# Kernel tuning notes

Hardware: AMD Instinct MI355X
Metric: run time of the kernel (lower is better)

## Reference

```python
import jax, jax.numpy as jnp
import numpy as np

H = 128  # hidden_size

def setup_inputs() -> dict:
    key = jax.random.key(0)
    ks = jax.random.split(key, 12)
    B, SEQ = 256, 1000
    static = jax.random.normal(ks[0], (B, 2, SEQ), jnp.float32)
    dynamic = jax.random.uniform(ks[1], (B, 2, SEQ), jnp.float32)
    # Encoder = 1x1 Conv1d(in_ch -> H): weight (H, in_ch), bias (H,)
    def xavier(k, shape):
        fan_in, fan_out = shape[1], shape[0]
        lim = np.sqrt(6.0 / (fan_in + fan_out)).astype(np.float32)
        return jax.random.uniform(k, shape, jnp.float32, -lim, lim)
    enc_s_w = xavier(ks[2], (H, 2)); enc_s_b = jnp.zeros((H,), jnp.float32)
    enc_d_w = xavier(ks[3], (H, 2)); enc_d_b = jnp.zeros((H,), jnp.float32)
    v = xavier(ks[4], (1, H))[0]                 # attention vector (H,)
    W = xavier(ks[5], (H, 3 * H))                # attention matrix (H, 3H)
    dense_w = xavier(ks[6], (H, 128)); dense_b = jnp.zeros((H,), jnp.float32)
    lin_w = xavier(ks[7], (1, H)); lin_b = jnp.zeros((1,), jnp.float32)
    return {"static": static, "dynamic": dynamic,
            "enc_s_w": enc_s_w, "enc_s_b": enc_s_b,
            "enc_d_w": enc_d_w, "enc_d_b": enc_d_b,
            "v": v, "W": W,
            "dense_w": dense_w, "dense_b": dense_b,
            "lin_w": lin_w, "lin_b": lin_b}


def reference(static, dynamic, enc_s_w, enc_s_b, enc_d_w, enc_d_b,
              v, W, dense_w, dense_b, lin_w, lin_b):
    B = static.shape[0]
    # 1x1-conv encoders (computed once; identical across loop iterations)
    e = jnp.einsum('hc,bcs->bhs', enc_s_w, static) + enc_s_b[None, :, None]   # (B,H,S)
    dyn_ld = jnp.broadcast_to(dynamic[:, 1:2, :], dynamic.shape)              # load channel expanded
    d = jnp.einsum('hc,bcs->bhs', enc_d_w, dyn_ld) + enc_d_b[None, :, None]   # (B,H,S)
    hy = jnp.zeros((B, H), static.dtype)
    for _ in range(3):  # fixed 3-step refinement loop
        hidden = jnp.concatenate(
            [e, d, jnp.broadcast_to(hy[:, :, None], e.shape)], axis=1)        # (B,3H,S)
        u = jnp.tanh(jnp.einsum('hk,bks->bhs', W, hidden))                    # (B,H,S)
        logit = jnp.einsum('h,bhs->bs', v, u)                                 # (B,S)
        prob = jax.nn.softmax(logit, axis=-1)
        hy = jnp.einsum('bs,bhs->bh', prob, e)                                # context update
    out = jax.nn.relu(hy @ dense_w.T + dense_b) @ lin_w.T + lin_b             # (B,1)
    return out
```

## Files before the change

kernel.cpp:

```cpp
#include <hip/hip_runtime.h>
#include <math.h>

#define HH 128
#define SS 1000
#define NT 1024
#define NW (NT / 64)
#define PCT 512

#define C1 2.8853900817779268f
#define C2 1.4426950408889634f

__global__ __launch_bounds__(PCT) void sc_precompute(
    const float* __restrict__ enc_s_w, const float* __restrict__ enc_s_b,
    const float* __restrict__ enc_d_w, const float* __restrict__ enc_d_b,
    const float* __restrict__ v, const float* __restrict__ W,
    float* __restrict__ ws) {
    __shared__ float part[7][4][HH];
    const int t = threadIdx.x;
    const int h = t & (HH - 1);
    const int q = t >> 7;
    const float4* W1 = (const float4*)(W + h * (3 * HH));
    const float4* W2 = (const float4*)(W + h * (3 * HH) + HH);
    const float4* W3 = (const float4*)(W + h * (3 * HH) + 2 * HH);
    const float4* ES = (const float4*)enc_s_w;
    const float4* ED = (const float4*)enc_d_w;
    const float4* SB = (const float4*)enc_s_b;
    const float4* DB = (const float4*)enc_d_b;
    float a0 = 0.f, a1 = 0.f, ad = 0.f, cc = 0.f, w30 = 0.f, w31 = 0.f, w3b = 0.f;
    #pragma unroll
    for (int k4 = q * 8; k4 < q * 8 + 8; ++k4) {
        float4 w1 = W1[k4], w2 = W2[k4], w3 = W3[k4];
        float4 e01 = ES[2 * k4], e23 = ES[2 * k4 + 1];
        float4 d01 = ED[2 * k4], d23 = ED[2 * k4 + 1];
        float4 sb = SB[k4], db = DB[k4];
        a0 = fmaf(w1.x, e01.x, a0); a0 = fmaf(w1.y, e01.z, a0);
        a0 = fmaf(w1.z, e23.x, a0); a0 = fmaf(w1.w, e23.z, a0);
        a1 = fmaf(w1.x, e01.y, a1); a1 = fmaf(w1.y, e01.w, a1);
        a1 = fmaf(w1.z, e23.y, a1); a1 = fmaf(w1.w, e23.w, a1);
        ad = fmaf(w2.x, d01.x + d01.y, ad); ad = fmaf(w2.y, d01.z + d01.w, ad);
        ad = fmaf(w2.z, d23.x + d23.y, ad); ad = fmaf(w2.w, d23.z + d23.w, ad);
        cc = fmaf(w1.x, sb.x, cc); cc = fmaf(w1.y, sb.y, cc);
        cc = fmaf(w1.z, sb.z, cc); cc = fmaf(w1.w, sb.w, cc);
        cc = fmaf(w2.x, db.x, cc); cc = fmaf(w2.y, db.y, cc);
        cc = fmaf(w2.z, db.z, cc); cc = fmaf(w2.w, db.w, cc);
        w30 = fmaf(w3.x, e01.x, w30); w30 = fmaf(w3.y, e01.z, w30);
        w30 = fmaf(w3.z, e23.x, w30); w30 = fmaf(w3.w, e23.z, w30);
        w31 = fmaf(w3.x, e01.y, w31); w31 = fmaf(w3.y, e01.w, w31);
        w31 = fmaf(w3.z, e23.y, w31); w31 = fmaf(w3.w, e23.w, w31);
        w3b = fmaf(w3.x, sb.x, w3b); w3b = fmaf(w3.y, sb.y, w3b);
        w3b = fmaf(w3.z, sb.z, w3b); w3b = fmaf(w3.w, sb.w, w3b);
    }
    part[0][q][h] = a0;  part[1][q][h] = a1;  part[2][q][h] = ad;
    part[3][q][h] = cc;  part[4][q][h] = w30; part[5][q][h] = w31;
    part[6][q][h] = w3b;
    __syncthreads();
    if (t < HH) {
        float r[7];
        #pragma unroll
        for (int i = 0; i < 7; ++i)
            r[i] = (part[i][0][t] + part[i][1][t]) + (part[i][2][t] + part[i][3][t]);
        ws[t]           = r[0] * C1;
        ws[HH + t]      = r[1] * C1;
        ws[2 * HH + t]  = r[2] * C1;
        ws[3 * HH + t]  = v[t];
        ws[4 * HH + t]  = r[3] * C1;
        ws[5 * HH + t]  = (r[3] + r[6]) * C1;
        ws[6 * HH + t]  = r[4] * C1;
        ws[7 * HH + t]  = r[5] * C1;
    }
    if (t == 0) {
        const float4* V4 = (const float4*)v;
        float s = 0.f;
        #pragma unroll 4
        for (int k = 0; k < HH / 4; ++k) { float4 x = V4[k]; s += x.x + x.y + x.z + x.w; }
        ws[8 * HH] = s * C2;
    }
}

template <int CTRL>
__device__ __forceinline__ float dpp_add(float x) {
    int s = __builtin_amdgcn_update_dpp(0, __builtin_bit_cast(int, x),
                                        CTRL, 0xF, 0xF, true);
    return x + __builtin_bit_cast(float, s);
}

__device__ __forceinline__ float grp4(float4 a0, float4 a1, float4 ad, float4 vv,
                                      float4 cg, float x0, float x1, float yv,
                                      float acc) {
    float z0 = fmaf(a0.x, x0, fmaf(a1.x, x1, fmaf(ad.x, yv, cg.x)));
    float z1 = fmaf(a0.y, x0, fmaf(a1.y, x1, fmaf(ad.y, yv, cg.y)));
    float z2 = fmaf(a0.z, x0, fmaf(a1.z, x1, fmaf(ad.z, yv, cg.z)));
    float z3 = fmaf(a0.w, x0, fmaf(a1.w, x1, fmaf(ad.w, yv, cg.w)));
    float e0 = __builtin_amdgcn_exp2f(z0);
    float e1 = __builtin_amdgcn_exp2f(z1);
    float e2 = __builtin_amdgcn_exp2f(z2);
    float e3 = __builtin_amdgcn_exp2f(z3);
    acc = fmaf(vv.x, __builtin_amdgcn_rcpf(1.f + e0), acc);
    acc = fmaf(vv.y, __builtin_amdgcn_rcpf(1.f + e1), acc);
    acc = fmaf(vv.z, __builtin_amdgcn_rcpf(1.f + e2), acc);
    acc = fmaf(vv.w, __builtin_amdgcn_rcpf(1.f + e3), acc);
    return acc;
}

__device__ __forceinline__ float4 bias4(float4 cb, float4 w0, float4 w1,
                                        float X0, float X1) {
    return make_float4(fmaf(w0.x, X0, fmaf(w1.x, X1, cb.x)),
                       fmaf(w0.y, X0, fmaf(w1.y, X1, cb.y)),
                       fmaf(w0.z, X0, fmaf(w1.z, X1, cb.z)),
                       fmaf(w0.w, X0, fmaf(w1.w, X1, cb.w)));
}

__global__ __launch_bounds__(NT) void sc_main(
    const float* __restrict__ stat, const float* __restrict__ dyn,
    const float* __restrict__ ws,
    const float* __restrict__ enc_s_w, const float* __restrict__ enc_s_b,
    const float* __restrict__ dense_w, const float* __restrict__ dense_b,
    const float* __restrict__ lin_w, const float* __restrict__ lin_b,
    float* __restrict__ out) {
    const int b    = blockIdx.x;
    const int t    = threadIdx.x;
    const int wave = t >> 6;
    const int lane = t & 63;
    const int g    = t & 15;
    const int sg   = t >> 4;

    __shared__ __align__(16) float4 xs[NT];
    __shared__ float4 red4[2][NW];
    __shared__ __align__(16) float hy_sh[HH];

    {
        float x0 = 0.f, x1 = 0.f, yv = 0.f;
        if (t < SS) {
            const float* sb = stat + (size_t)b * 2 * SS;
            x0 = sb[t];
            x1 = sb[SS + t];
            yv = dyn[(size_t)b * 2 * SS + SS + t];
        }
        xs[t] = make_float4(x0, x1, yv, 0.f);
    }

    const float* wp = ws + g * 8;
    const float4 a0L = *(const float4*)(wp);
    const float4 a0H = *(const float4*)(wp + 4);
    const float4 a1L = *(const float4*)(wp + HH);
    const float4 a1H = *(const float4*)(wp + HH + 4);
    const float4 adL = *(const float4*)(wp + 2 * HH);
    const float4 adH = *(const float4*)(wp + 2 * HH + 4);
    const float4 vvL = *(const float4*)(wp + 3 * HH);
    const float4 vvH = *(const float4*)(wp + 3 * HH + 4);
    const float4 c0L = *(const float4*)(wp + 4 * HH);
    const float4 c0H = *(const float4*)(wp + 4 * HH + 4);
    const float4 cbL = *(const float4*)(wp + 5 * HH);
    const float4 cbH = *(const float4*)(wp + 5 * HH + 4);
    const float4 w0L = *(const float4*)(wp + 6 * HH);
    const float4 w0H = *(const float4*)(wp + 6 * HH + 4);
    const float4 w1L = *(const float4*)(wp + 7 * HH);
    const float4 w1H = *(const float4*)(wp + 7 * HH + 4);
    const float svc2 = ws[8 * HH];

    __syncthreads();

    float X0 = 0.f, X1 = 0.f;

    auto run_iter = [&](float4 cgL, float4 cgH, int parity) {
        float S = 0.f, Sx0 = 0.f, Sx1 = 0.f;
        for (int pass = 0; pass < 16; ++pass) {
            const int s = pass * 64 + sg;
            float4 x = xs[s];
            float acc = grp4(a0L, a1L, adL, vvL, cgL, x.x, x.y, x.z, 0.f);
            acc = grp4(a0H, a1H, adH, vvH, cgH, x.x, x.y, x.z, acc);
            acc = dpp_add<0x118>(acc);
            acc = dpp_add<0x114>(acc);
            acc = dpp_add<0x112>(acc);
            acc = dpp_add<0x111>(acc);
            const bool own = (g == 15) && (s < SS);
            float arg = own ? fmaf(-C1, acc, svc2) : -200.f;
            float p = __builtin_amdgcn_exp2f(arg);
            S   += p;
            Sx0  = fmaf(p, x.x, Sx0);
            Sx1  = fmaf(p, x.y, Sx1);
        }
        S   += __shfl_xor(S, 16);   S   += __shfl_xor(S, 32);
        Sx0 += __shfl_xor(Sx0, 16); Sx0 += __shfl_xor(Sx0, 32);
        Sx1 += __shfl_xor(Sx1, 16); Sx1 += __shfl_xor(Sx1, 32);
        if (lane == 15) red4[parity][wave] = make_float4(S, Sx0, Sx1, 0.f);
        __syncthreads();
        float4 w4 = red4[parity][lane & 15];
        #pragma unroll
        for (int off = 1; off < 16; off <<= 1) {
            w4.x += __shfl_xor(w4.x, off);
            w4.y += __shfl_xor(w4.y, off);
            w4.z += __shfl_xor(w4.z, off);
        }
        float inv = __builtin_amdgcn_rcpf(w4.x);
        X0 = w4.y * inv;
        X1 = w4.z * inv;
    };

    run_iter(c0L, c0H, 0);
    run_iter(bias4(cbL, w0L, w1L, X0, X1), bias4(cbH, w0H, w1H, X0, X1), 1);
    run_iter(bias4(cbL, w0L, w1L, X0, X1), bias4(cbH, w0H, w1H, X0, X1), 0);

    if (t < HH)
        hy_sh[t] = fmaf(enc_s_w[2 * t], X0, fmaf(enc_s_w[2 * t + 1], X1, enc_s_b[t]));
    __syncthreads();

    float o = 0.f;
    if (t < HH) {
        const float4* dw4 = (const float4*)(dense_w + t * HH);
        const float4* hy4 = (const float4*)hy_sh;
        float r = dense_b[t];
        #pragma unroll 4
        for (int k = 0; k < HH / 4; ++k) {
            float4 d4 = dw4[k], h4 = hy4[k];
            r = fmaf(d4.x, h4.x, fmaf(d4.y, h4.y, fmaf(d4.z, h4.z, fmaf(d4.w, h4.w, r))));
        }
        o = lin_w[t] * fmaxf(r, 0.f);
    }
    #pragma unroll
    for (int off = 32; off > 0; off >>= 1) o += __shfl_xor(o, off);
    if (lane == 0) red4[0][wave].x = o;
    __syncthreads();
    if (t == 0) {
        float s = 0.f;
        for (int i = 0; i < NW; ++i) s += red4[0][i].x;
        out[b] = s + lin_b[0];
    }
}

extern "C" void kernel_launch(void* const* d_in, const int* in_sizes, int n_in,
                              void* d_out, int out_size, void* d_ws, size_t ws_size,
                              hipStream_t stream) {
    const float* stat    = (const float*)d_in[0];
    const float* dyn     = (const float*)d_in[1];
    const float* enc_s_w = (const float*)d_in[2];
    const float* enc_s_b = (const float*)d_in[3];
    const float* enc_d_w = (const float*)d_in[4];
    const float* enc_d_b = (const float*)d_in[5];
    const float* v       = (const float*)d_in[6];
    const float* W       = (const float*)d_in[7];
    const float* dense_w = (const float*)d_in[8];
    const float* dense_b = (const float*)d_in[9];
    const float* lin_w   = (const float*)d_in[10];
    const float* lin_b   = (const float*)d_in[11];
    float* out = (float*)d_out;
    float* ws  = (float*)d_ws;

    const int B = in_sizes[0] / (2 * SS);

    hipLaunchKernelGGL(sc_precompute, dim3(1), dim3(PCT), 0, stream,
                       enc_s_w, enc_s_b, enc_d_w, enc_d_b, v, W, ws);
    hipLaunchKernelGGL(sc_main, dim3(B), dim3(NT), 0, stream,
                       stat, dyn, ws, enc_s_w, enc_s_b, dense_w, dense_b,
                       lin_w, lin_b, out);
}
```

Measured before the change: 50.80 us.

## Fuse weight precompute into main kernel and pin folded constants in registers

After: 47.96 us. 1.06x faster.

```diff
diff --git a/kernel.cpp b/kernel.cpp
--- a/kernel.cpp
+++ b/kernel.cpp
@@ -5,77 +5,11 @@
 #define SS 1000
 #define NT 1024
 #define NW (NT / 64)
-#define PCT 512
 
 #define C1 2.8853900817779268f
 #define C2 1.4426950408889634f
 
-__global__ __launch_bounds__(PCT) void sc_precompute(
-    const float* __restrict__ enc_s_w, const float* __restrict__ enc_s_b,
-    const float* __restrict__ enc_d_w, const float* __restrict__ enc_d_b,
-    const float* __restrict__ v, const float* __restrict__ W,
-    float* __restrict__ ws) {
-    __shared__ float part[7][4][HH];
-    const int t = threadIdx.x;
-    const int h = t & (HH - 1);
-    const int q = t >> 7;
-    const float4* W1 = (const float4*)(W + h * (3 * HH));
-    const float4* W2 = (const float4*)(W + h * (3 * HH) + HH);
-    const float4* W3 = (const float4*)(W + h * (3 * HH) + 2 * HH);
-    const float4* ES = (const float4*)enc_s_w;
-    const float4* ED = (const float4*)enc_d_w;
-    const float4* SB = (const float4*)enc_s_b;
-    const float4* DB = (const float4*)enc_d_b;
-    float a0 = 0.f, a1 = 0.f, ad = 0.f, cc = 0.f, w30 = 0.f, w31 = 0.f, w3b = 0.f;
-    #pragma unroll
-    for (int k4 = q * 8; k4 < q * 8 + 8; ++k4) {
-        float4 w1 = W1[k4], w2 = W2[k4], w3 = W3[k4];
-        float4 e01 = ES[2 * k4], e23 = ES[2 * k4 + 1];
-        float4 d01 = ED[2 * k4], d23 = ED[2 * k4 + 1];
-        float4 sb = SB[k4], db = DB[k4];
-        a0 = fmaf(w1.x, e01.x, a0); a0 = fmaf(w1.y, e01.z, a0);
-        a0 = fmaf(w1.z, e23.x, a0); a0 = fmaf(w1.w, e23.z, a0);
-        a1 = fmaf(w1.x, e01.y, a1); a1 = fmaf(w1.y, e01.w, a1);
-        a1 = fmaf(w1.z, e23.y, a1); a1 = fmaf(w1.w, e23.w, a1);
-        ad = fmaf(w2.x, d01.x + d01.y, ad); ad = fmaf(w2.y, d01.z + d01.w, ad);
-        ad = fmaf(w2.z, d23.x + d23.y, ad); ad = fmaf(w2.w, d23.z + d23.w, ad);
-        cc = fmaf(w1.x, sb.x, cc); cc = fmaf(w1.y, sb.y, cc);
-        cc = fmaf(w1.z, sb.z, cc); cc = fmaf(w1.w, sb.w, cc);
-        cc = fmaf(w2.x, db.x, cc); cc = fmaf(w2.y, db.y, cc);
-        cc = fmaf(w2.z, db.z, cc); cc = fmaf(w2.w, db.w, cc);
-        w30 = fmaf(w3.x, e01.x, w30); w30 = fmaf(w3.y, e01.z, w30);
-        w30 = fmaf(w3.z, e23.x, w30); w30 = fmaf(w3.w, e23.z, w30);
-        w31 = fmaf(w3.x, e01.y, w31); w31 = fmaf(w3.y, e01.w, w31);
-        w31 = fmaf(w3.z, e23.y, w31); w31 = fmaf(w3.w, e23.w, w31);
-        w3b = fmaf(w3.x, sb.x, w3b); w3b = fmaf(w3.y, sb.y, w3b);
-        w3b = fmaf(w3.z, sb.z, w3b); w3b = fmaf(w3.w, sb.w, w3b);
-    }
-    part[0][q][h] = a0;  part[1][q][h] = a1;  part[2][q][h] = ad;
-    part[3][q][h] = cc;  part[4][q][h] = w30; part[5][q][h] = w31;
-    part[6][q][h] = w3b;
-    __syncthreads();
-    if (t < HH) {
-        float r[7];
-        #pragma unroll
-        for (int i = 0; i < 7; ++i)
-            r[i] = (part[i][0][t] + part[i][1][t]) + (part[i][2][t] + part[i][3][t]);
-        ws[t]           = r[0] * C1;
-        ws[HH + t]      = r[1] * C1;
-        ws[2 * HH + t]  = r[2] * C1;
-        ws[3 * HH + t]  = v[t];
-        ws[4 * HH + t]  = r[3] * C1;
-        ws[5 * HH + t]  = (r[3] + r[6]) * C1;
-        ws[6 * HH + t]  = r[4] * C1;
-        ws[7 * HH + t]  = r[5] * C1;
-    }
-    if (t == 0) {
-        const float4* V4 = (const float4*)v;
-        float s = 0.f;
-        #pragma unroll 4
-        for (int k = 0; k < HH / 4; ++k) { float4 x = V4[k]; s += x.x + x.y + x.z + x.w; }
-        ws[8 * HH] = s * C2;
-    }
-}
+__device__ __forceinline__ void pin(float& x) { asm volatile("" : "+v"(x)); }
 
 template <int CTRL>
 __device__ __forceinline__ float dpp_add(float x) {
@@ -84,36 +18,11 @@
     return x + __builtin_bit_cast(float, s);
 }
 
-__device__ __forceinline__ float grp4(float4 a0, float4 a1, float4 ad, float4 vv,
-                                      float4 cg, float x0, float x1, float yv,
-                                      float acc) {
-    float z0 = fmaf(a0.x, x0, fmaf(a1.x, x1, fmaf(ad.x, yv, cg.x)));
-    float z1 = fmaf(a0.y, x0, fmaf(a1.y, x1, fmaf(ad.y, yv, cg.y)));
-    float z2 = fmaf(a0.z, x0, fmaf(a1.z, x1, fmaf(ad.z, yv, cg.z)));
-    float z3 = fmaf(a0.w, x0, fmaf(a1.w, x1, fmaf(ad.w, yv, cg.w)));
-    float e0 = __builtin_amdgcn_exp2f(z0);
-    float e1 = __builtin_amdgcn_exp2f(z1);
-    float e2 = __builtin_amdgcn_exp2f(z2);
-    float e3 = __builtin_amdgcn_exp2f(z3);
-    acc = fmaf(vv.x, __builtin_amdgcn_rcpf(1.f + e0), acc);
-    acc = fmaf(vv.y, __builtin_amdgcn_rcpf(1.f + e1), acc);
-    acc = fmaf(vv.z, __builtin_amdgcn_rcpf(1.f + e2), acc);
-    acc = fmaf(vv.w, __builtin_amdgcn_rcpf(1.f + e3), acc);
-    return acc;
-}
-
-__device__ __forceinline__ float4 bias4(float4 cb, float4 w0, float4 w1,
-                                        float X0, float X1) {
-    return make_float4(fmaf(w0.x, X0, fmaf(w1.x, X1, cb.x)),
-                       fmaf(w0.y, X0, fmaf(w1.y, X1, cb.y)),
-                       fmaf(w0.z, X0, fmaf(w1.z, X1, cb.z)),
-                       fmaf(w0.w, X0, fmaf(w1.w, X1, cb.w)));
-}
-
-__global__ __launch_bounds__(NT) void sc_main(
+__global__ __launch_bounds__(NT, 4) void sc_fused(
     const float* __restrict__ stat, const float* __restrict__ dyn,
-    const float* __restrict__ ws,
     const float* __restrict__ enc_s_w, const float* __restrict__ enc_s_b,
+    const float* __restrict__ enc_d_w, const float* __restrict__ enc_d_b,
+    const float* __restrict__ v, const float* __restrict__ W,
     const float* __restrict__ dense_w, const float* __restrict__ dense_b,
     const float* __restrict__ lin_w, const float* __restrict__ lin_b,
     float* __restrict__ out) {
@@ -124,9 +33,12 @@
     const int g    = t & 15;
     const int sg   = t >> 4;
 
+    __shared__ float part[7][8][HH];
     __shared__ __align__(16) float4 xs[NT];
+    __shared__ __align__(16) float kc[8][HH];
     __shared__ float4 red4[2][NW];
-    __shared__ __align__(16) float hy_sh[HH];
+    __shared__ float hy_sh[HH];
+    __shared__ float svc2_sh;
 
     {
         float x0 = 0.f, x1 = 0.f, yv = 0.f;
@@ -139,36 +51,147 @@
         xs[t] = make_float4(x0, x1, yv, 0.f);
     }
 
-    const float* wp = ws + g * 8;
-    const float4 a0L = *(const float4*)(wp);
-    const float4 a0H = *(const float4*)(wp + 4);
-    const float4 a1L = *(const float4*)(wp + HH);
-    const float4 a1H = *(const float4*)(wp + HH + 4);
-    const float4 adL = *(const float4*)(wp + 2 * HH);
-    const float4 adH = *(const float4*)(wp + 2 * HH + 4);
-    const float4 vvL = *(const float4*)(wp + 3 * HH);
-    const float4 vvH = *(const float4*)(wp + 3 * HH + 4);
-    const float4 c0L = *(const float4*)(wp + 4 * HH);
-    const float4 c0H = *(const float4*)(wp + 4 * HH + 4);
-    const float4 cbL = *(const float4*)(wp + 5 * HH);
-    const float4 cbH = *(const float4*)(wp + 5 * HH + 4);
-    const float4 w0L = *(const float4*)(wp + 6 * HH);
-    const float4 w0H = *(const float4*)(wp + 6 * HH + 4);
-    const float4 w1L = *(const float4*)(wp + 7 * HH);
-    const float4 w1H = *(const float4*)(wp + 7 * HH + 4);
-    const float svc2 = ws[8 * HH];
-
-    __syncthreads();
+    {
+        const int h = t & (HH - 1);
+        const int q = t >> 7;
+        const float4* W1 = (const float4*)(W + h * (3 * HH));
+        const float4* W2 = (const float4*)(W + h * (3 * HH) + HH);
+        const float4* W3 = (const float4*)(W + h * (3 * HH) + 2 * HH);
+        const float4* ES = (const float4*)enc_s_w;
+        const float4* ED = (const float4*)enc_d_w;
+        const float4* SB = (const float4*)enc_s_b;
+        const float4* DB = (const float4*)enc_d_b;
+        float a0 = 0.f, a1 = 0.f, ad = 0.f, cc = 0.f, w30 = 0.f, w31 = 0.f, w3b = 0.f;
+        #pragma unroll
+        for (int k4 = q * 4; k4 < q * 4 + 4; ++k4) {
+            float4 w1 = W1[k4], w2 = W2[k4], w3 = W3[k4];
+            float4 e01 = ES[2 * k4], e23 = ES[2 * k4 + 1];
+            float4 d01 = ED[2 * k4], d23 = ED[2 * k4 + 1];
+            float4 sb = SB[k4], db = DB[k4];
+            a0 = fmaf(w1.x, e01.x, a0); a0 = fmaf(w1.y, e01.z, a0);
+            a0 = fmaf(w1.z, e23.x, a0); a0 = fmaf(w1.w, e23.z, a0);
+            a1 = fmaf(w1.x, e01.y, a1); a1 = fmaf(w1.y, e01.w, a1);
+            a1 = fmaf(w1.z, e23.y, a1); a1 = fmaf(w1.w, e23.w, a1);
+            ad = fmaf(w2.x, d01.x + d01.y, ad); ad = fmaf(w2.y, d01.z + d01.w, ad);
+            ad = fmaf(w2.z, d23.x + d23.y, ad); ad = fmaf(w2.w, d23.z + d23.w, ad);
+            cc = fmaf(w1.x, sb.x, cc); cc = fmaf(w1.y, sb.y, cc);
+            cc = fmaf(w1.z, sb.z, cc); cc = fmaf(w1.w, sb.w, cc);
+            cc = fmaf(w2.x, db.x, cc); cc = fmaf(w2.y, db.y, cc);
+            cc = fmaf(w2.z, db.z, cc); cc = fmaf(w2.w, db.w, cc);
+            w30 = fmaf(w3.x, e01.x, w30); w30 = fmaf(w3.y, e01.z, w30);
+            w30 = fmaf(w3.z, e23.x, w30); w30 = fmaf(w3.w, e23.z, w30);
+            w31 = fmaf(w3.x, e01.y, w31); w31 = fmaf(w3.y, e01.w, w31);
+            w31 = fmaf(w3.z, e23.y, w31); w31 = fmaf(w3.w, e23.w, w31);
+            w3b = fmaf(w3.x, sb.x, w3b); w3b = fmaf(w3.y, sb.y, w3b);
+            w3b = fmaf(w3.z, sb.z, w3b); w3b = fmaf(w3.w, sb.w, w3b);
+        }
+        part[0][q][h] = a0;  part[1][q][h] = a1;  part[2][q][h] = ad;
+        part[3][q][h] = cc;  part[4][q][h] = w30; part[5][q][h] = w31;
+        part[6][q][h] = w3b;
+    }
+    __syncthreads();
+
+    if (t < HH) {
+        float r0 = 0.f, r1 = 0.f, r2 = 0.f, r3 = 0.f, r4 = 0.f, r5 = 0.f, r6 = 0.f;
+        #pragma unroll
+        for (int q = 0; q < 8; ++q) {
+            r0 += part[0][q][t]; r1 += part[1][q][t]; r2 += part[2][q][t];
+            r3 += part[3][q][t]; r4 += part[4][q][t]; r5 += part[5][q][t];
+            r6 += part[6][q][t];
+        }
+        kc[0][t] = r0 * C1;
+        kc[1][t] = r1 * C1;
+        kc[2][t] = r2 * C1;
+        kc[3][t] = v[t];
+        kc[4][t] = r3 * C1;
+        kc[5][t] = (r3 + r6) * C1;
+        kc[6][t] = r4 * C1;
+        kc[7][t] = r5 * C1;
+    } else if (t < 160) {
+        int j = t - 128;
+        float4 x = ((const float4*)v)[j];
+        float s = (x.x + x.y) + (x.z + x.w);
+        #pragma unroll
+        for (int off = 1; off < 32; off <<= 1) s += __shfl_xor(s, off);
+        if (t == 128) svc2_sh = s * C2;
+    }
+    __syncthreads();
+
+    const int h0 = g * 8;
+    float4 f;
+    f = *(const float4*)&kc[0][h0];     float a00 = f.x, a01 = f.y, a02 = f.z, a03 = f.w;
+    f = *(const float4*)&kc[0][h0 + 4]; float a04 = f.x, a05 = f.y, a06 = f.z, a07 = f.w;
+    f = *(const float4*)&kc[1][h0];     float a10 = f.x, a11 = f.y, a12 = f.z, a13 = f.w;
+    f = *(const float4*)&kc[1][h0 + 4]; float a14 = f.x, a15 = f.y, a16 = f.z, a17 = f.w;
+    f = *(const float4*)&kc[2][h0];     float ad0 = f.x, ad1 = f.y, ad2 = f.z, ad3 = f.w;
+    f = *(const float4*)&kc[2][h0 + 4]; float ad4 = f.x, ad5 = f.y, ad6 = f.z, ad7 = f.w;
+    f = *(const float4*)&kc[3][h0];     float vv0 = f.x, vv1 = f.y, vv2 = f.z, vv3 = f.w;
+    f = *(const float4*)&kc[3][h0 + 4]; float vv4 = f.x, vv5 = f.y, vv6 = f.z, vv7 = f.w;
+    pin(a00); pin(a01); pin(a02); pin(a03); pin(a04); pin(a05); pin(a06); pin(a07);
+    pin(a10); pin(a11); pin(a12); pin(a13); pin(a14); pin(a15); pin(a16); pin(a17);
+    pin(ad0); pin(ad1); pin(ad2); pin(ad3); pin(ad4); pin(ad5); pin(ad6); pin(ad7);
+    pin(vv0); pin(vv1); pin(vv2); pin(vv3); pin(vv4); pin(vv5); pin(vv6); pin(vv7);
+    float svc2 = svc2_sh;
+    pin(svc2);
 
     float X0 = 0.f, X1 = 0.f;
 
-    auto run_iter = [&](float4 cgL, float4 cgH, int parity) {
+    auto run_iter = [&](int iter, int parity) {
+        float cg0, cg1, cg2, cg3, cg4, cg5, cg6, cg7;
+        if (iter == 0) {
+            float4 lo = *(const float4*)&kc[4][h0];
+            float4 hi = *(const float4*)&kc[4][h0 + 4];
+            cg0 = lo.x; cg1 = lo.y; cg2 = lo.z; cg3 = lo.w;
+            cg4 = hi.x; cg5 = hi.y; cg6 = hi.z; cg7 = hi.w;
+        } else {
+            float4 cbl = *(const float4*)&kc[5][h0];
+            float4 cbh = *(const float4*)&kc[5][h0 + 4];
+            float4 w0l = *(const float4*)&kc[6][h0];
+            float4 w0h = *(const float4*)&kc[6][h0 + 4];
+            float4 w1l = *(const float4*)&kc[7][h0];
+            float4 w1h = *(const float4*)&kc[7][h0 + 4];
+            cg0 = fmaf(w0l.x, X0, fmaf(w1l.x, X1, cbl.x));
+            cg1 = fmaf(w0l.y, X0, fmaf(w1l.y, X1, cbl.y));
+            cg2 = fmaf(w0l.z, X0, fmaf(w1l.z, X1, cbl.z));
+            cg3 = fmaf(w0l.w, X0, fmaf(w1l.w, X1, cbl.w));
+            cg4 = fmaf(w0h.x, X0, fmaf(w1h.x, X1, cbh.x));
+            cg5 = fmaf(w0h.y, X0, fmaf(w1h.y, X1, cbh.y));
+            cg6 = fmaf(w0h.z, X0, fmaf(w1h.z, X1, cbh.z));
+            cg7 = fmaf(w0h.w, X0, fmaf(w1h.w, X1, cbh.w));
+        }
+        pin(cg0); pin(cg1); pin(cg2); pin(cg3);
+        pin(cg4); pin(cg5); pin(cg6); pin(cg7);
+
         float S = 0.f, Sx0 = 0.f, Sx1 = 0.f;
+        #pragma unroll 4
         for (int pass = 0; pass < 16; ++pass) {
             const int s = pass * 64 + sg;
             float4 x = xs[s];
-            float acc = grp4(a0L, a1L, adL, vvL, cgL, x.x, x.y, x.z, 0.f);
-            acc = grp4(a0H, a1H, adH, vvH, cgH, x.x, x.y, x.z, acc);
+            float z0 = fmaf(a00, x.x, fmaf(a10, x.y, fmaf(ad0, x.z, cg0)));
+            float z1 = fmaf(a01, x.x, fmaf(a11, x.y, fmaf(ad1, x.z, cg1)));
+            float z2 = fmaf(a02, x.x, fmaf(a12, x.y, fmaf(ad2, x.z, cg2)));
+            float z3 = fmaf(a03, x.x, fmaf(a13, x.y, fmaf(ad3, x.z, cg3)));
+            float z4 = fmaf(a04, x.x, fmaf(a14, x.y, fmaf(ad4, x.z, cg4)));
+            float z5 = fmaf(a05, x.x, fmaf(a15, x.y, fmaf(ad5, x.z, cg5)));
+            float z6 = fmaf(a06, x.x, fmaf(a16, x.y, fmaf(ad6, x.z, cg6)));
+            float z7 = fmaf(a07, x.x, fmaf(a17, x.y, fmaf(ad7, x.z, cg7)));
+            float e0 = __builtin_amdgcn_exp2f(z0);
+            float e1 = __builtin_amdgcn_exp2f(z1);
+            float e2 = __builtin_amdgcn_exp2f(z2);
+            float e3 = __builtin_amdgcn_exp2f(z3);
+            float e4 = __builtin_amdgcn_exp2f(z4);
+            float e5 = __builtin_amdgcn_exp2f(z5);
+            float e6 = __builtin_amdgcn_exp2f(z6);
+            float e7 = __builtin_amdgcn_exp2f(z7);
+            float acc;
+            acc = fmaf(vv0, __builtin_amdgcn_rcpf(1.f + e0), 0.f);
+            acc = fmaf(vv1, __builtin_amdgcn_rcpf(1.f + e1), acc);
+            acc = fmaf(vv2, __builtin_amdgcn_rcpf(1.f + e2), acc);
+            acc = fmaf(vv3, __builtin_amdgcn_rcpf(1.f + e3), acc);
+            acc = fmaf(vv4, __builtin_amdgcn_rcpf(1.f + e4), acc);
+            acc = fmaf(vv5, __builtin_amdgcn_rcpf(1.f + e5), acc);
+            acc = fmaf(vv6, __builtin_amdgcn_rcpf(1.f + e6), acc);
+            acc = fmaf(vv7, __builtin_amdgcn_rcpf(1.f + e7), acc);
             acc = dpp_add<0x118>(acc);
             acc = dpp_add<0x114>(acc);
             acc = dpp_add<0x112>(acc);
@@ -197,9 +220,9 @@
         X1 = w4.z * inv;
     };
 
-    run_iter(c0L, c0H, 0);
-    run_iter(bias4(cbL, w0L, w1L, X0, X1), bias4(cbH, w0H, w1H, X0, X1), 1);
-    run_iter(bias4(cbL, w0L, w1L, X0, X1), bias4(cbH, w0H, w1H, X0, X1), 0);
+    run_iter(0, 0);
+    run_iter(1, 1);
+    run_iter(2, 0);
 
     if (t < HH)
         hy_sh[t] = fmaf(enc_s_w[2 * t], X0, fmaf(enc_s_w[2 * t + 1], X1, enc_s_b[t]));
@@ -244,13 +267,10 @@
     const float* lin_w   = (const float*)d_in[10];
     const float* lin_b   = (const float*)d_in[11];
     float* out = (float*)d_out;
-    float* ws  = (float*)d_ws;
 
     const int B = in_sizes[0] / (2 * SS);
 
-    hipLaunchKernelGGL(sc_precompute, dim3(1), dim3(PCT), 0, stream,
-                       enc_s_w, enc_s_b, enc_d_w, enc_d_b, v, W, ws);
-    hipLaunchKernelGGL(sc_main, dim3(B), dim3(NT), 0, stream,
-                       stat, dyn, ws, enc_s_w, enc_s_b, dense_w, dense_b,
-                       lin_w, lin_b, out);
+    hipLaunchKernelGGL(sc_fused, dim3(B), dim3(NT), 0, stream,
+                       stat, dyn, enc_s_w, enc_s_b, enc_d_w, enc_d_b, v, W,
+                       dense_w, dense_b, lin_w, lin_b, out);
 }
```
